# Kernel tuning notes

Hardware: AMD Instinct MI355X
Metric: run time of the kernel (lower is better)

The kernel has to match this reference:

```python
import jax, jax.numpy as jnp
import numpy as np

H = 8          # num heads
D = 16         # head dim
HID = 128      # hidden_dim = H * D
NM, ND, NA = 100000, 20000, 50000
E = 300000     # edges per relation
NUM_CLASSES = 8


def setup_inputs() -> dict:
    key = jax.random.key(0)
    ks = jax.random.split(key, 24)
    s = 0.05
    eye = jnp.eye(D, dtype=jnp.float32)
    inp = {
        'x_movie': jax.random.normal(ks[0], (NM, 256), jnp.float32),
        'x_director': jax.random.normal(ks[1], (ND, 128), jnp.float32),
        'x_actor': jax.random.normal(ks[2], (NA, 128), jnp.float32),
        # edge lists per relation: (director->movie, actor->movie, movie->director, movie->actor)
        'src_dm': jax.random.randint(ks[3], (E,), 0, ND),
        'dst_dm': jax.random.randint(ks[4], (E,), 0, NM),
        'src_am': jax.random.randint(ks[5], (E,), 0, NA),
        'dst_am': jax.random.randint(ks[6], (E,), 0, NM),
        'src_md': jax.random.randint(ks[7], (E,), 0, NM),
        'dst_md': jax.random.randint(ks[8], (E,), 0, ND),
        'src_ma': jax.random.randint(ks[9], (E,), 0, NM),
        'dst_ma': jax.random.randint(ks[10], (E,), 0, NA),
        # per-type pre-encoder (use_pre_encoder=True)
        'Wpre_m': jax.random.normal(ks[11], (256, HID), jnp.float32) * s,
        'Wpre_d': jax.random.normal(ks[12], (128, HID), jnp.float32) * s,
        'Wpre_a': jax.random.normal(ks[13], (128, HID), jnp.float32) * s,
        'bpre': jnp.zeros((3, HID), jnp.float32),
        # per-type K/Q/V projections, stacked over the 3 node types
        'Wk': jax.random.normal(ks[14], (3, HID, HID), jnp.float32) * s,
        'bk': jnp.zeros((3, HID), jnp.float32),
        'Wq': jax.random.normal(ks[15], (3, HID, HID), jnp.float32) * s,
        'bq': jnp.zeros((3, HID), jnp.float32),
        'Wv': jax.random.normal(ks[16], (3, HID, HID), jnp.float32) * s,
        'bv': jnp.zeros((3, HID), jnp.float32),
        # per-relation attention / message matrices and priors (4 relations)
        'a_rel': eye + jax.random.normal(ks[17], (4, H, D, D), jnp.float32) * s,
        'm_rel': eye + jax.random.normal(ks[18], (4, H, D, D), jnp.float32) * s,
        'p_rel': jnp.ones((4, H), jnp.float32),
        # per-type skip gate and output projection
        'skip': jnp.ones((3,), jnp.float32),
        'Wa': jax.random.normal(ks[19], (3, HID, HID), jnp.float32) * s,
        'ba': jnp.zeros((3, HID), jnp.float32),
        # final classification head on target node type ('movie')
        'Wlin': jax.random.normal(ks[20], (HID, NUM_CLASSES), jnp.float32) * s,
        'blin': jnp.zeros((NUM_CLASSES,), jnp.float32),
    }
    return inp


def _seg_softmax_agg(alpha, msg, dst, n):
    # softmax over incoming edges of each destination node, then weighted sum of msgs
    m = jax.ops.segment_max(alpha, dst, num_segments=n)      # [n, H]
    m = jnp.where(jnp.isfinite(m), m, 0.0)
    a = jnp.exp(alpha - m[dst])                              # [E, H]
    denom = jax.ops.segment_sum(a, dst, num_segments=n)      # [n, H]
    num = jax.ops.segment_sum(a[:, :, None] * msg, dst, num_segments=n)  # [n, H, D]
    return num / jnp.maximum(denom, 1e-16)[:, :, None]


def reference(x_movie, x_director, x_actor,
              src_dm, dst_dm, src_am, dst_am, src_md, dst_md, src_ma, dst_ma,
              Wpre_m, Wpre_d, Wpre_a, bpre, Wk, bk, Wq, bq, Wv, bv,
              a_rel, m_rel, p_rel, skip, Wa, ba, Wlin, blin):
    # type order: 0=movie, 1=director, 2=actor
    xs = [x_movie @ Wpre_m + bpre[0],
          x_director @ Wpre_d + bpre[1],
          x_actor @ Wpre_a + bpre[2]]
    k = [(x @ Wk[t] + bk[t]).reshape(-1, H, D) for t, x in enumerate(xs)]
    q = [(x @ Wq[t] + bq[t]).reshape(-1, H, D) for t, x in enumerate(xs)]
    v = [(x @ Wv[t] + bv[t]).reshape(-1, H, D) for t, x in enumerate(xs)]

    # (src_type, dst_type, src_idx, dst_idx) per relation
    rels = [(1, 0, src_dm, dst_dm), (2, 0, src_am, dst_am),
            (0, 1, src_md, dst_md), (0, 2, src_ma, dst_ma)]
    scale = 1.0 / np.sqrt(D).astype(np.float32)
    buckets = {0: [], 1: [], 2: []}
    for r, (st, dt, src, dst) in enumerate(rels):
        ke = jnp.einsum('ehd,hdf->ehf', k[st][src], a_rel[r])          # [E,H,D]
        al = jnp.einsum('ehf,ehf->eh', q[dt][dst], ke) * p_rel[r] * scale
        me = jnp.einsum('ehd,hdf->ehf', v[st][src], m_rel[r])          # [E,H,D]
        buckets[dt].append((al, me, dst))

    n = [x.shape[0] for x in xs]
    outs = []
    for t in range(3):
        al = jnp.concatenate([b[0] for b in buckets[t]], axis=0)
        me = jnp.concatenate([b[1] for b in buckets[t]], axis=0)
        dst = jnp.concatenate([b[2] for b in buckets[t]], axis=0)
        agg = _seg_softmax_agg(al, me, dst, n[t]).reshape(n[t], HID)
        h = jax.nn.gelu(agg, approximate=False) @ Wa[t] + ba[t]
        g = jax.nn.sigmoid(skip[t])
        outs.append(g * h + (1.0 - g) * xs[t])

    return outs[0] @ Wlin + blin
```

## Files before the change

### kernel.cpp

```cpp
#include <hip/hip_runtime.h>
#include <hip/hip_bf16.h>
#include <math.h>

#define NM 100000
#define ND 20000
#define NA 50000
#define EDG 300000
#define CAP 32

#define NT_M   3125
#define NT_D   625
#define NT_K   2188
#define T_M    7
#define T_K    7
#define BLK_M  447
#define BLK_K  313

typedef __attribute__((ext_vector_type(8))) short shortx8;
typedef __attribute__((ext_vector_type(4))) float floatx4;
typedef __attribute__((ext_vector_type(4))) int intx4;

__device__ __forceinline__ float bf2f(unsigned int u) {
    return __uint_as_float(u << 16);
}
__device__ __forceinline__ unsigned short f2bf(float f) {
    unsigned int x = __float_as_uint(f);
    unsigned int r = x + 0x7fffu + ((x >> 16) & 1u);
    return (unsigned short)(r >> 16);
}
__device__ __forceinline__ unsigned short f2bf_fast(float f) {
    return (unsigned short)((__float_as_uint(f) + 0x8000u) >> 16);
}
__device__ __forceinline__ unsigned int pkbf2(float a, float b) {
    return __builtin_amdgcn_perm(__float_as_uint(b) + 0x8000u,
                                 __float_as_uint(a) + 0x8000u,
                                 0x07060302u);
}
__device__ __forceinline__ float gelu_exact(float x) {
    return 0.5f * x * (1.0f + erff(x * 0.70710678118654752f));
}

static const size_t OFF_BT_Q      = 0;
static const size_t OFF_BT_KAMV_D = 73728;
static const size_t OFF_BT_KAMV_A = 139264;
static const size_t OFF_WKA_D     = 204800;
static const size_t OFF_WVM_D     = 270336;
static const size_t OFF_WKA_A     = 335872;
static const size_t OFF_WVM_A     = 401408;
static const size_t OFF_BQ        = 466944;
static const size_t OFF_B_KAMV_D  = 467520;
static const size_t OFF_B_KAMV_A  = 468544;
static const size_t OFF_BKA_D     = 469568;
static const size_t OFF_BVM_D     = 470080;
static const size_t OFF_BKA_A     = 470592;
static const size_t OFF_BVM_A     = 471104;
static const size_t OFF_WALS      = 471616;
static const size_t OFF_BFIN      = 475712;
static const size_t OFF_Q0        = 524288;
static const size_t OFF_SKIPB     = 26124288;
static const size_t OFF_WQT       = 26124288;
static const size_t OFF_KAMV_D    = 29324288;
static const size_t OFF_KAMV_A    = 39564288;
static const size_t OFF_COUNTS    = 65164288;
static const size_t OFF_SLOTS     = 65564288;
#define KAMV_A_DELTA 10240000

__global__ __launch_bounds__(256) void precompA(
    const float* __restrict__ Wk, const float* __restrict__ bk,
    const float* __restrict__ Wv, const float* __restrict__ bv,
    const float* __restrict__ Wa, const float* __restrict__ ba,
    const float* __restrict__ Wlin, const float* __restrict__ blin,
    const float* __restrict__ a_rel, const float* __restrict__ m_rel,
    const float* __restrict__ p_rel, const float* __restrict__ skip,
    const float* __restrict__ bpre, const float* __restrict__ Wq,
    char* __restrict__ ws)
{
    int tid = blockIdx.x * 256 + threadIdx.x;
    if (tid < 65536) {
        int mat = tid >> 14, rem = tid & 16383;
        int e = rem >> 7, hf = rem & 127, h = hf >> 4, f = hf & 15;
        const float* Wsrc; const float* R; float sc; float* dst;
        if (mat == 0)      { Wsrc = Wk + 16384; R = a_rel;        sc = p_rel[h]     * 0.25f; dst = (float*)(ws + OFF_WKA_D); }
        else if (mat == 1) { Wsrc = Wv + 16384; R = m_rel;        sc = 1.0f;                 dst = (float*)(ws + OFF_WVM_D); }
        else if (mat == 2) { Wsrc = Wk + 32768; R = a_rel + 2048; sc = p_rel[8 + h] * 0.25f; dst = (float*)(ws + OFF_WKA_A); }
        else               { Wsrc = Wv + 32768; R = m_rel + 2048; sc = 1.0f;                 dst = (float*)(ws + OFF_WVM_A); }
        float s = 0.0f;
        for (int d = 0; d < 16; d++)
            s += Wsrc[e * 128 + h * 16 + d] * R[h * 256 + d * 16 + f];
        dst[hf * 128 + e] = s * sc;
    } else if (tid < 66048) {
        int idx = tid - 65536;
        int mat = idx >> 7, hf = idx & 127, h = hf >> 4, f = hf & 15;
        const float* bsrc; const float* R; float sc; float* dst;
        if (mat == 0)      { bsrc = bk + 128; R = a_rel;        sc = p_rel[h]     * 0.25f; dst = (float*)(ws + OFF_BKA_D); }
        else if (mat == 1) { bsrc = bv + 128; R = m_rel;        sc = 1.0f;                 dst = (float*)(ws + OFF_BVM_D); }
        else if (mat == 2) { bsrc = bk + 256; R = a_rel + 2048; sc = p_rel[8 + h] * 0.25f; dst = (float*)(ws + OFF_BKA_A); }
        else               { bsrc = bv + 256; R = m_rel + 2048; sc = 1.0f;                 dst = (float*)(ws + OFF_BVM_A); }
        float s = 0.0f;
        for (int d = 0; d < 16; d++)
            s += bsrc[h * 16 + d] * R[h * 256 + d * 16 + f];
        dst[hf] = s * sc;
    } else if (tid < 67072) {
        int idx = tid - 66048;
        int j = idx >> 3, c = idx & 7;
        float g = 1.0f / (1.0f + __expf(-skip[0]));
        float s = 0.0f;
        for (int o = 0; o < 128; o++)
            s += Wa[j * 128 + o] * Wlin[o * 8 + c];
        ((float*)(ws + OFF_WALS))[j * 8 + c] = g * s;
    } else if (tid < 67080) {
        int c = tid - 67072;
        float g = 1.0f / (1.0f + __expf(-skip[0]));
        float s1 = 0.0f, s2 = 0.0f;
        for (int o = 0; o < 128; o++) {
            s1 += ba[o]   * Wlin[o * 8 + c];
            s2 += bpre[o] * Wlin[o * 8 + c];
        }
        ((float*)(ws + OFF_BFIN))[c] = g * s1 + (1.0f - g) * s2 + blin[c];
    } else if (tid < 83464) {
        int i = tid - 67080;
        int n = i >> 7, e = i & 127;
        ((float*)(ws + OFF_WQT))[n * 128 + e] = Wq[e * 128 + n];
    } else if (tid < 83464 + NM) {
        ((int*)(ws + OFF_COUNTS))[tid - 83464] = 0;
    }
}

__device__ __forceinline__ float dot128(const float* __restrict__ a,
                                        const float* __restrict__ b) {
    const floatx4* x = (const floatx4*)a;
    const floatx4* y = (const floatx4*)b;
    float s = 0.0f;
    #pragma unroll
    for (int i = 0; i < 32; i++) {
        floatx4 u = x[i], v = y[i];
        s += u[0] * v[0] + u[1] * v[1] + u[2] * v[2] + u[3] * v[3];
    }
    return s;
}

__global__ __launch_bounds__(256) void prep_scat(
    const int* __restrict__ src_dm, const int* __restrict__ dst_dm,
    const int* __restrict__ src_am, const int* __restrict__ dst_am,
    const float* __restrict__ Wpre_m, const float* __restrict__ Wpre_d,
    const float* __restrict__ Wpre_a, const float* __restrict__ bpre,
    const float* __restrict__ bq, const float* __restrict__ Wlin,
    const float* __restrict__ skip,
    char* __restrict__ ws)
{
    if (blockIdx.x < 2344) {
        int t = blockIdx.x * 256 + threadIdx.x;
        if (t >= 2 * EDG) return;
        int src, dst, delta;
        if (t < EDG) { src = src_dm[t];       dst = dst_dm[t];       delta = 0; }
        else         { src = src_am[t - EDG]; dst = dst_am[t - EDG]; delta = KAMV_A_DELTA; }
        int* counts = (int*)(ws + OFF_COUNTS);
        int* slots  = (int*)(ws + OFF_SLOTS);
        int pos = atomicAdd(&counts[dst], 1);
        if (pos < CAP) slots[(size_t)dst * CAP + pos] = src * 512 + delta;
        return;
    }
    int tid = (blockIdx.x - 2344) * 256 + threadIdx.x;
    const float* WKA_D = (const float*)(ws + OFF_WKA_D);
    const float* WVM_D = (const float*)(ws + OFF_WVM_D);
    const float* WKA_A = (const float*)(ws + OFF_WKA_A);
    const float* WVM_A = (const float*)(ws + OFF_WVM_A);
    const float* WqT   = (const float*)(ws + OFF_WQT);

    if (tid < 36864) {
        int n = tid >> 8, c = tid & 255;
        float s = 0.0f;
        if (n < 128) {
            s = dot128(Wpre_m + c * 128, WqT + n * 128);
        } else if (n < 136) {
            int cc = n - 128;
            float g = 1.0f / (1.0f + __expf(-skip[0]));
            for (int e = 0; e < 128; e++)
                s += Wpre_m[c * 128 + e] * Wlin[e * 8 + cc];
            s *= (1.0f - g);
        }
        ((unsigned short*)(ws + OFF_BT_Q))[(c >> 7) * 18432 + n * 128 + (c & 127)] = f2bf(s);
    } else if (tid < 69632) {
        int idx = tid - 36864;
        int nrow = idx >> 7, c = idx & 127;
        const float* WfT = (nrow < 128) ? WKA_D : WVM_D;
        int nc = nrow & 127;
        float s = dot128(Wpre_d + c * 128, WfT + nc * 128);
        ((unsigned short*)(ws + OFF_BT_KAMV_D))[nrow * 128 + c] = f2bf(s);
    } else if (tid < 102400) {
        int idx = tid - 69632;
        int nrow = idx >> 7, c = idx & 127;
        const float* WfT = (nrow < 128) ? WKA_A : WVM_A;
        int nc = nrow & 127;
        float s = dot128(Wpre_a + c * 128, WfT + nc * 128);
        ((unsigned short*)(ws + OFF_BT_KAMV_A))[nrow * 128 + c] = f2bf(s);
    } else if (tid < 102544) {
        int n = tid - 102400;
        float s = 0.0f;
        if (n < 128) s = dot128(bpre, WqT + n * 128) + bq[n];
        ((float*)(ws + OFF_BQ))[n] = s;
    } else if (tid < 102800) {
        int nrow = tid - 102544;
        const float* WfT = (nrow < 128) ? WKA_D : WVM_D;
        const float* bf_ = (nrow < 128) ? (const float*)(ws + OFF_BKA_D) : (const float*)(ws + OFF_BVM_D);
        int nc = nrow & 127;
        ((float*)(ws + OFF_B_KAMV_D))[nrow] = dot128(bpre + 128, WfT + nc * 128) + bf_[nc];
    } else if (tid < 103056) {
        int nrow = tid - 102800;
        const float* WfT = (nrow < 128) ? WKA_A : WVM_A;
        const float* bf_ = (nrow < 128) ? (const float*)(ws + OFF_BKA_A) : (const float*)(ws + OFF_BVM_A);
        int nc = nrow & 127;
        ((float*)(ws + OFF_B_KAMV_A))[nrow] = dot128(bpre + 256, WfT + nc * 128) + bf_[nc];
    }
}

#define MFMA16(a, b, c) __builtin_amdgcn_mfma_f32_16x16x32_bf16(a, b, c, 0, 0, 0)

__global__ __launch_bounds__(256, 3) void gemm_all(
    const float* __restrict__ xm, const float* __restrict__ xd,
    const float* __restrict__ xa,
    const unsigned short* __restrict__ btq,
    const unsigned short* __restrict__ btd,
    const unsigned short* __restrict__ bta,
    const float* __restrict__ bq,
    const float* __restrict__ bbd, const float* __restrict__ bba,
    unsigned short* __restrict__ q0, float* __restrict__ skipb,
    unsigned short* __restrict__ outd, unsigned short* __restrict__ outa)
{
    __shared__ unsigned short a_lds[32 * 136];
    __shared__ unsigned short b_lds[144 * 136];
    int tid = threadIdx.x;
    int w = tid >> 6, lane = tid & 63;
    int quad = lane >> 4, low = lane & 15;
    int g = w >> 1, s = w & 1;
    int bx = blockIdx.x;

    if (bx < BLK_M) {
        int tbase = bx * T_M;
        floatx4 av[4];
        intx4 bv[9];
        {
            int row0 = (tbase < NT_M ? tbase : NT_M - 1) * 32;
            #pragma unroll
            for (int it = 0; it < 4; it++) {
                int f = it * 256 + tid, r = f >> 5, c4 = f & 31;
                av[it] = *(const floatx4*)(xm + (size_t)(row0 + r) * 256 + c4 * 4);
            }
            #pragma unroll
            for (int it = 0; it < 9; it++) {
                int idx = it * 256 + tid, n = idx >> 4, ch = idx & 15;
                bv[it] = *(const intx4*)&btq[(size_t)n * 128 + ch * 8];
            }
        }
        for (int t = 0; t < T_M; t++) {
            int tcur = tbase + t;
            if (tcur >= NT_M) break;
            int row0 = tcur * 32;
            floatx4 acc[5] = {};
            #pragma unroll
            for (int h = 0; h < 2; h++) {
                __syncthreads();
                #pragma unroll
                for (int it = 0; it < 4; it++) {
                    int f = it * 256 + tid, r = f >> 5, c4 = f & 31;
                    unsigned long long d =
                        ((unsigned long long)pkbf2(av[it][2], av[it][3]) << 32) |
                        pkbf2(av[it][0], av[it][1]);
                    *(unsigned long long*)&a_lds[r * 136 + c4 * 4] = d;
                }
                #pragma unroll
                for (int it = 0; it < 9; it++) {
                    int idx = it * 256 + tid, n = idx >> 4, ch = idx & 15;
                    *(intx4*)&b_lds[n * 136 + ch * 8] = bv[it];
                }
                __syncthreads();
                {
                    int ntile = (h == 0) ? tcur : (tcur + 1 < NT_M ? tcur + 1 : NT_M - 1);
                    int nh = 1 - h;
                    int nrow0 = ntile * 32;
                    #pragma unroll
                    for (int it = 0; it < 4; it++) {
                        int f = it * 256 + tid, r = f >> 5, c4 = f & 31;
                        av[it] = *(const floatx4*)(xm + (size_t)(nrow0 + r) * 256 + nh * 128 + c4 * 4);
                    }
                    #pragma unroll
                    for (int it = 0; it < 9; it++) {
                        int idx = it * 256 + tid, n = idx >> 4, ch = idx & 15;
                        bv[it] = *(const intx4*)&btq[(size_t)nh * 18432 + n * 128 + ch * 8];
                    }
                }
                #pragma unroll
                for (int ks = 0; ks < 4; ks++) {
                    int ko = ks * 32 + quad * 8;
                    shortx8 a0 = *(const shortx8*)&a_lds[(s * 16 + low) * 136 + ko];
                    #pragma unroll
                    for (int j = 0; j < 5; j++) {
                        if (g == 1 && j == 4) continue;
                        int nt = g * 5 + j;
                        shortx8 b = *(const shortx8*)&b_lds[(nt * 16 + low) * 136 + ko];
                        acc[j] = MFMA16(a0, b, acc[j]);
                    }
                }
            }
            #pragma unroll
            for (int j = 0; j < 5; j++) {
                if (g == 1 && j == 4) continue;
                int nt = g * 5 + j;
                int col = nt * 16 + low;
                #pragma unroll
                for (int r = 0; r < 4; r++) {
                    int row = row0 + s * 16 + quad * 4 + r;
                    float v = acc[j][r] + bq[col];
                    if (nt == 8) {
                        if (low < 8) skipb[(size_t)row * 8 + low] = v;
                    } else {
                        q0[(size_t)row * 128 + col] = f2bf_fast(v);
                    }
                }
            }
        }
    } else {
        int kbase = (bx - BLK_M) * T_K;
        floatx4 av[4];
        intx4 bv[8];
        {
            int tt = kbase < NT_K ? kbase : NT_K - 1;
            const float* A; int M, row0;
            const unsigned short* BT;
            if (tt < NT_D) { A = xd; M = ND; row0 = tt * 32; BT = btd; }
            else           { A = xa; M = NA; row0 = (tt - NT_D) * 32; BT = bta; }
            #pragma unroll
            for (int it = 0; it < 4; it++) {
                int f = it * 256 + tid, r = f >> 5, c4 = f & 31;
                int rg = row0 + r; if (rg >= M) rg = M - 1;
                av[it] = *(const floatx4*)(A + (size_t)rg * 128 + c4 * 4);
            }
            #pragma unroll
            for (int it = 0; it < 8; it++) {
                int idx = it * 256 + tid, n = idx >> 4, ch = idx & 15;
                bv[it] = *(const intx4*)&BT[(size_t)n * 128 + ch * 8];
            }
        }
        for (int t = 0; t < T_K; t++) {
            int tcur = kbase + t;
            if (tcur >= NT_K) break;
            const float* A; int M, row0;
            const unsigned short* BT; const float* bias;
            unsigned short* outb;
            if (tcur < NT_D) { A = xd; M = ND; row0 = tcur * 32; BT = btd; bias = bbd; outb = outd; }
            else             { A = xa; M = NA; row0 = (tcur - NT_D) * 32; BT = bta; bias = bba; outb = outa; }

            #pragma unroll
            for (int pnl = 0; pnl < 2; pnl++) {
                __syncthreads();
                if (pnl == 0) {
                    #pragma unroll
                    for (int it = 0; it < 4; it++) {
                        int f = it * 256 + tid, r = f >> 5, c4 = f & 31;
                        unsigned long long d =
                            ((unsigned long long)pkbf2(av[it][2], av[it][3]) << 32) |
                            pkbf2(av[it][0], av[it][1]);
                        *(unsigned long long*)&a_lds[r * 136 + c4 * 4] = d;
                    }
                }
                #pragma unroll
                for (int it = 0; it < 8; it++) {
                    int idx = it * 256 + tid, n = idx >> 4, ch = idx & 15;
                    *(intx4*)&b_lds[n * 136 + ch * 8] = bv[it];
                }
                __syncthreads();
                if (pnl == 0) {
                    #pragma unroll
                    for (int it = 0; it < 8; it++) {
                        int idx = it * 256 + tid, n = idx >> 4, ch = idx & 15;
                        bv[it] = *(const intx4*)&BT[16384 + (size_t)n * 128 + ch * 8];
                    }
                } else {
                    int tn = (tcur + 1 < NT_K) ? tcur + 1 : NT_K - 1;
                    const float* An; int Mn, nrow0;
                    const unsigned short* BTn;
                    if (tn < NT_D) { An = xd; Mn = ND; nrow0 = tn * 32; BTn = btd; }
                    else           { An = xa; Mn = NA; nrow0 = (tn - NT_D) * 32; BTn = bta; }
                    #pragma unroll
                    for (int it = 0; it < 4; it++) {
                        int f = it * 256 + tid, r = f >> 5, c4 = f & 31;
                        int rg = nrow0 + r; if (rg >= Mn) rg = Mn - 1;
                        av[it] = *(const floatx4*)(An + (size_t)rg * 128 + c4 * 4);
                    }
                    #pragma unroll
                    for (int it = 0; it < 8; it++) {
                        int idx = it * 256 + tid, n = idx >> 4, ch = idx & 15;
                        bv[it] = *(const intx4*)&BTn[(size_t)n * 128 + ch * 8];
                    }
                }
                floatx4 acc[4] = {};
                #pragma unroll
                for (int ks = 0; ks < 4; ks++) {
                    int ko = ks * 32 + quad * 8;
                    shortx8 a0 = *(const shortx8*)&a_lds[(s * 16 + low) * 136 + ko];
                    #pragma unroll
                    for (int j = 0; j < 4; j++) {
                        int nt = g * 4 + j;
                        shortx8 b = *(const shortx8*)&b_lds[(nt * 16 + low) * 136 + ko];
                        acc[j] = MFMA16(a0, b, acc[j]);
                    }
                }
                #pragma unroll
                for (int j = 0; j < 4; j++) {
                    int nt = g * 4 + j;
                    int col = pnl * 128 + nt * 16 + low;
                    #pragma unroll
                    for (int r = 0; r < 4; r++) {
                        int row = row0 + s * 16 + quad * 4 + r;
                        if (row < M)
                            outb[(size_t)row * 256 + col] = f2bf_fast(acc[j][r] + bias[pnl * 128 + nt * 16 + low]);
                    }
                }
            }
        }
    }
}

__global__ __launch_bounds__(256) void agg_kernel(
    const unsigned short* __restrict__ q0,
    const char* __restrict__ kamv0,
    const int* __restrict__ counts, const int* __restrict__ slots,
    const float* __restrict__ skipb,
    const float* __restrict__ WaLs, const float* __restrict__ bfin,
    float* __restrict__ out)
{
    __shared__ float wals[1032];
    for (int i = threadIdx.x; i < 1024; i += 256) {
        int c = i >> 7, rem = i & 127, j = rem >> 4, L = rem & 15;
        wals[i] = WaLs[(L * 8 + j) * 8 + c];
    }
    if (threadIdx.x < 8) wals[1024 + threadIdx.x] = bfin[threadIdx.x];
    __syncthreads();

    int lane = threadIdx.x & 63;
    int grp = lane >> 4;
    int L   = lane & 15;
    int n = blockIdx.x * 16 + (threadIdx.x >> 6) * 4 + grp;

    intx4 qv = *(const intx4*)(q0 + (size_t)n * 128 + L * 8);
    float qf[8];
    #pragma unroll
    for (int d = 0; d < 4; d++) {
        unsigned int u = (unsigned int)qv[d];
        qf[2 * d]     = __uint_as_float(u << 16);
        qf[2 * d + 1] = __uint_as_float(u & 0xffff0000u);
    }

    int cnt = counts[n];
    cnt = cnt < 0 ? 0 : (cnt > CAP ? CAP : cnt);
    int s0 = slots[(size_t)n * CAP + L];

    float acc[8] = {0, 0, 0, 0, 0, 0, 0, 0};
    float den = 0.0f;
    if (cnt > 0) {
        int off0 = __shfl(s0, lane & 48);
        const char* p = kamv0 + off0;
        intx4 ku = *(const intx4*)(p + L * 16);
        intx4 mu = *(const intx4*)(p + 256 + L * 16);
        for (int i = 0; i < cnt; i++) {
            int inext = (i + 1 < cnt) ? i + 1 : i;
            int offn = __shfl(s0, (lane & 48) + (inext & 15));
            if (__builtin_expect(inext >= 16, 0)) offn = slots[(size_t)n * CAP + inext];
            const char* pn = kamv0 + offn;
            intx4 kun = *(const intx4*)(pn + L * 16);
            intx4 mun = *(const intx4*)(pn + 256 + L * 16);

            float ph = 0.0f;
            #pragma unroll
            for (int d = 0; d < 4; d++) {
                unsigned int u = (unsigned int)ku[d];
                ph += qf[2 * d]     * __uint_as_float(u << 16);
                ph += qf[2 * d + 1] * __uint_as_float(u & 0xffff0000u);
            }
            float pf = ph + __shfl_xor(ph, 1);
            float wgt = __expf(fminf(pf, 60.0f));
            den += wgt;
            #pragma unroll
            for (int d = 0; d < 4; d++) {
                unsigned int u = (unsigned int)mu[d];
                acc[2 * d]     += wgt * __uint_as_float(u << 16);
                acc[2 * d + 1] += wgt * __uint_as_float(u & 0xffff0000u);
            }
            ku = kun; mu = mun;
        }
    }
    float inv = 1.0f / fmaxf(den, 1e-16f);

    float part[8] = {0, 0, 0, 0, 0, 0, 0, 0};
    #pragma unroll
    for (int j = 0; j < 8; j++) {
        float u = gelu_exact(acc[j] * inv);
        #pragma unroll
        for (int c = 0; c < 8; c++)
            part[c] += u * wals[c * 128 + j * 16 + L];
    }

    bool b0 = lane & 1, b1 = lane & 2, b2 = lane & 4;
    float t1[4], t2[2], t3;
    #pragma unroll
    for (int k = 0; k < 4; k++) {
        float send = b0 ? part[k] : part[4 + k];
        float got  = __shfl_xor(send, 1);
        t1[k] = (b0 ? part[4 + k] : part[k]) + got;
    }
    #pragma unroll
    for (int k = 0; k < 2; k++) {
        float send = b1 ? t1[k] : t1[2 + k];
        float got  = __shfl_xor(send, 2);
        t2[k] = (b1 ? t1[2 + k] : t1[k]) + got;
    }
    {
        float send = b2 ? t2[0] : t2[1];
        float got  = __shfl_xor(send, 4);
        t3 = (b2 ? t2[1] : t2[0]) + got;
    }
    t3 += __shfl_xor(t3, 8);
    if (L < 8) {
        int c = 4 * (L & 1) + 2 * ((L >> 1) & 1) + ((L >> 2) & 1);
        out[(size_t)n * 8 + c] = t3 + skipb[(size_t)n * 8 + c] + wals[1024 + c];
    }
}

extern "C" void kernel_launch(void* const* d_in, const int* in_sizes, int n_in,
                              void* d_out, int out_size, void* d_ws, size_t ws_size,
                              hipStream_t stream) {
    (void)in_sizes; (void)n_in; (void)out_size; (void)ws_size;
    const float* x_movie    = (const float*)d_in[0];
    const float* x_director = (const float*)d_in[1];
    const float* x_actor    = (const float*)d_in[2];
    const int* src_dm = (const int*)d_in[3];
    const int* dst_dm = (const int*)d_in[4];
    const int* src_am = (const int*)d_in[5];
    const int* dst_am = (const int*)d_in[6];
    const float* Wpre_m = (const float*)d_in[11];
    const float* Wpre_d = (const float*)d_in[12];
    const float* Wpre_a = (const float*)d_in[13];
    const float* bpre   = (const float*)d_in[14];
    const float* Wk     = (const float*)d_in[15];
    const float* bk     = (const float*)d_in[16];
    const float* Wq     = (const float*)d_in[17];
    const float* bq     = (const float*)d_in[18];
    const float* Wv     = (const float*)d_in[19];
    const float* bv     = (const float*)d_in[20];
    const float* a_rel  = (const float*)d_in[21];
    const float* m_rel  = (const float*)d_in[22];
    const float* p_rel  = (const float*)d_in[23];
    const float* skip   = (const float*)d_in[24];
    const float* Wa     = (const float*)d_in[25];
    const float* ba     = (const float*)d_in[26];
    const float* Wlin   = (const float*)d_in[27];
    const float* blin   = (const float*)d_in[28];

    char* ws = (char*)d_ws;
    float* out = (float*)d_out;

    precompA<<<(83464 + NM + 255) / 256, 256, 0, stream>>>(
        Wk, bk, Wv, bv, Wa, ba, Wlin, blin,
        a_rel, m_rel, p_rel, skip, bpre, Wq, ws);

    prep_scat<<<2344 + 403, 256, 0, stream>>>(
        src_dm, dst_dm, src_am, dst_am,
        Wpre_m, Wpre_d, Wpre_a, bpre, bq, Wlin, skip, ws);

    gemm_all<<<BLK_M + BLK_K, 256, 0, stream>>>(
        x_movie, x_director, x_actor,
        (const unsigned short*)(ws + OFF_BT_Q),
        (const unsigned short*)(ws + OFF_BT_KAMV_D),
        (const unsigned short*)(ws + OFF_BT_KAMV_A),
        (const float*)(ws + OFF_BQ),
        (const float*)(ws + OFF_B_KAMV_D), (const float*)(ws + OFF_B_KAMV_A),
        (unsigned short*)(ws + OFF_Q0), (float*)(ws + OFF_SKIPB),
        (unsigned short*)(ws + OFF_KAMV_D), (unsigned short*)(ws + OFF_KAMV_A));

    agg_kernel<<<NM / 16, 256, 0, stream>>>(
        (const unsigned short*)(ws + OFF_Q0),
        (const char*)(ws + OFF_KAMV_D),
        (const int*)(ws + OFF_COUNTS), (const int*)(ws + OFF_SLOTS),
        (const float*)(ws + OFF_SKIPB),
        (const float*)(ws + OFF_WALS), (const float*)(ws + OFF_BFIN), out);
}
```

Before: 402.2 us.

## Keep full weight matrix resident in LDS and feed A fragments from registers

The projection GEMM now loads the entire bf16 weight panel into shared memory once per block. Each wave then independently processes four 16-row tiles, loading A rows straight from global memory into registers, packing them to bf16 and feeding the MFMA without staging through LDS. This removes the per-tile barriers and LDS writes of A and re-staging of B, and register prefetch of the next tile overlaps loads with compute. The cost is a larger LDS footprint and more registers (occupancy hint lowered from 3 to 2), and the director and actor blocks are now split statically.

```diff
diff --git a/kernel.cpp b/kernel.cpp
--- a/kernel.cpp
+++ b/kernel.cpp
@@ -8,13 +8,12 @@
 #define EDG 300000
 #define CAP 32
 
-#define NT_M   3125
-#define NT_D   625
-#define NT_K   2188
-#define T_M    7
-#define T_K    7
-#define BLK_M  447
-#define BLK_K  313
+#define NTM 6250
+#define NTD 1250
+#define NTA 3125
+#define MB  391
+#define DB  79
+#define AB  196
 
 typedef __attribute__((ext_vector_type(8))) short shortx8;
 typedef __attribute__((ext_vector_type(4))) float floatx4;
@@ -35,6 +34,14 @@
     return __builtin_amdgcn_perm(__float_as_uint(b) + 0x8000u,
                                  __float_as_uint(a) + 0x8000u,
                                  0x07060302u);
+}
+__device__ __forceinline__ shortx8 pack8(floatx4 a, floatx4 b) {
+    intx4 r;
+    r[0] = (int)pkbf2(a[0], a[1]);
+    r[1] = (int)pkbf2(a[2], a[3]);
+    r[2] = (int)pkbf2(b[0], b[1]);
+    r[3] = (int)pkbf2(b[2], b[3]);
+    return __builtin_bit_cast(shortx8, r);
 }
 __device__ __forceinline__ float gelu_exact(float x) {
     return 0.5f * x * (1.0f + erff(x * 0.70710678118654752f));
@@ -216,7 +223,7 @@
 
 #define MFMA16(a, b, c) __builtin_amdgcn_mfma_f32_16x16x32_bf16(a, b, c, 0, 0, 0)
 
-__global__ __launch_bounds__(256, 3) void gemm_all(
+__global__ __launch_bounds__(256, 2) void gemm_all(
     const float* __restrict__ xm, const float* __restrict__ xd,
     const float* __restrict__ xa,
     const unsigned short* __restrict__ btq,
@@ -227,194 +234,136 @@
     unsigned short* __restrict__ q0, float* __restrict__ skipb,
     unsigned short* __restrict__ outd, unsigned short* __restrict__ outa)
 {
-    __shared__ unsigned short a_lds[32 * 136];
-    __shared__ unsigned short b_lds[144 * 136];
+    __shared__ unsigned short b_lds[288 * 136];
     int tid = threadIdx.x;
     int w = tid >> 6, lane = tid & 63;
     int quad = lane >> 4, low = lane & 15;
-    int g = w >> 1, s = w & 1;
     int bx = blockIdx.x;
 
-    if (bx < BLK_M) {
-        int tbase = bx * T_M;
-        floatx4 av[4];
-        intx4 bv[9];
+    if (bx < MB) {
+        #pragma unroll
+        for (int it = 0; it < 18; it++) {
+            int idx = it * 256 + tid, r = idx >> 4, ch = idx & 15;
+            *(intx4*)&b_lds[r * 136 + ch * 8] =
+                *(const intx4*)&btq[(size_t)r * 128 + ch * 8];
+        }
+        __syncthreads();
+        float bqr[9];
+        #pragma unroll
+        for (int j = 0; j < 9; j++) bqr[j] = bq[j * 16 + low];
+
+        int t0 = (bx * 4 + w) * 4;
+        floatx4 st[16];
         {
-            int row0 = (tbase < NT_M ? tbase : NT_M - 1) * 32;
-            #pragma unroll
-            for (int it = 0; it < 4; it++) {
-                int f = it * 256 + tid, r = f >> 5, c4 = f & 31;
-                av[it] = *(const floatx4*)(xm + (size_t)(row0 + r) * 256 + c4 * 4);
-            }
-            #pragma unroll
-            for (int it = 0; it < 9; it++) {
-                int idx = it * 256 + tid, n = idx >> 4, ch = idx & 15;
-                bv[it] = *(const intx4*)&btq[(size_t)n * 128 + ch * 8];
-            }
-        }
-        for (int t = 0; t < T_M; t++) {
-            int tcur = tbase + t;
-            if (tcur >= NT_M) break;
-            int row0 = tcur * 32;
-            floatx4 acc[5] = {};
-            #pragma unroll
-            for (int h = 0; h < 2; h++) {
-                __syncthreads();
+            int te = t0 < NTM ? t0 : NTM - 1;
+            const float* Ap = xm + (size_t)(te * 16 + low) * 256 + quad * 8;
+            #pragma unroll
+            for (int ks = 0; ks < 8; ks++) {
+                st[2 * ks]     = *(const floatx4*)(Ap + ks * 32);
+                st[2 * ks + 1] = *(const floatx4*)(Ap + ks * 32 + 4);
+            }
+        }
+        #pragma unroll
+        for (int i = 0; i < 4; i++) {
+            int t = t0 + i;
+            shortx8 fa[8];
+            #pragma unroll
+            for (int ks = 0; ks < 8; ks++) fa[ks] = pack8(st[2 * ks], st[2 * ks + 1]);
+            {
+                int tn = t + 1 < NTM ? t + 1 : NTM - 1;
+                const float* Ap = xm + (size_t)(tn * 16 + low) * 256 + quad * 8;
                 #pragma unroll
-                for (int it = 0; it < 4; it++) {
-                    int f = it * 256 + tid, r = f >> 5, c4 = f & 31;
-                    unsigned long long d =
-                        ((unsigned long long)pkbf2(av[it][2], av[it][3]) << 32) |
-                        pkbf2(av[it][0], av[it][1]);
-                    *(unsigned long long*)&a_lds[r * 136 + c4 * 4] = d;
-                }
+                for (int ks = 0; ks < 8; ks++) {
+                    st[2 * ks]     = *(const floatx4*)(Ap + ks * 32);
+                    st[2 * ks + 1] = *(const floatx4*)(Ap + ks * 32 + 4);
+                }
+            }
+            floatx4 acc[9] = {};
+            #pragma unroll
+            for (int ks = 0; ks < 8; ks++) {
+                int rb = (ks >> 2) * 19584 + low * 136 + (ks & 3) * 32 + quad * 8;
                 #pragma unroll
-                for (int it = 0; it < 9; it++) {
-                    int idx = it * 256 + tid, n = idx >> 4, ch = idx & 15;
-                    *(intx4*)&b_lds[n * 136 + ch * 8] = bv[it];
-                }
-                __syncthreads();
-                {
-                    int ntile = (h == 0) ? tcur : (tcur + 1 < NT_M ? tcur + 1 : NT_M - 1);
-                    int nh = 1 - h;
-                    int nrow0 = ntile * 32;
+                for (int j = 0; j < 9; j++) {
+                    shortx8 b = *(const shortx8*)&b_lds[rb + j * 2176];
+                    acc[j] = MFMA16(fa[ks], b, acc[j]);
+                }
+            }
+            if (t < NTM) {
+                int row0 = t * 16 + quad * 4;
+                #pragma unroll
+                for (int j = 0; j < 8; j++) {
+                    int col = j * 16 + low;
                     #pragma unroll
-                    for (int it = 0; it < 4; it++) {
-                        int f = it * 256 + tid, r = f >> 5, c4 = f & 31;
-                        av[it] = *(const floatx4*)(xm + (size_t)(nrow0 + r) * 256 + nh * 128 + c4 * 4);
-                    }
+                    for (int r = 0; r < 4; r++)
+                        q0[(size_t)(row0 + r) * 128 + col] = f2bf_fast(acc[j][r] + bqr[j]);
+                }
+                if (low < 8) {
                     #pragma unroll
-                    for (int it = 0; it < 9; it++) {
-                        int idx = it * 256 + tid, n = idx >> 4, ch = idx & 15;
-                        bv[it] = *(const intx4*)&btq[(size_t)nh * 18432 + n * 128 + ch * 8];
-                    }
-                }
+                    for (int r = 0; r < 4; r++)
+                        skipb[(size_t)(row0 + r) * 8 + low] = acc[8][r] + bqr[8];
+                }
+            }
+        }
+    } else {
+        const float* A; const unsigned short* BT; const float* bias;
+        unsigned short* outb; int ntt, wid;
+        if (bx < MB + DB) { A = xd; BT = btd; bias = bbd; outb = outd; ntt = NTD; wid = (bx - MB) * 4 + w; }
+        else              { A = xa; BT = bta; bias = bba; outb = outa; ntt = NTA; wid = (bx - MB - DB) * 4 + w; }
+        #pragma unroll
+        for (int it = 0; it < 16; it++) {
+            int idx = it * 256 + tid, r = idx >> 4, ch = idx & 15;
+            *(intx4*)&b_lds[r * 136 + ch * 8] =
+                *(const intx4*)&BT[(size_t)r * 128 + ch * 8];
+        }
+        __syncthreads();
+        float biasr[16];
+        #pragma unroll
+        for (int j = 0; j < 16; j++) biasr[j] = bias[j * 16 + low];
+
+        int t0 = wid * 4;
+        floatx4 st[8];
+        {
+            int te = t0 < ntt ? t0 : ntt - 1;
+            const float* Ap = A + (size_t)(te * 16 + low) * 128 + quad * 8;
+            #pragma unroll
+            for (int ks = 0; ks < 4; ks++) {
+                st[2 * ks]     = *(const floatx4*)(Ap + ks * 32);
+                st[2 * ks + 1] = *(const floatx4*)(Ap + ks * 32 + 4);
+            }
+        }
+        #pragma unroll
+        for (int i = 0; i < 4; i++) {
+            int t = t0 + i;
+            shortx8 fa[4];
+            #pragma unroll
+            for (int ks = 0; ks < 4; ks++) fa[ks] = pack8(st[2 * ks], st[2 * ks + 1]);
+            {
+                int tn = t + 1 < ntt ? t + 1 : ntt - 1;
+                const float* Ap = A + (size_t)(tn * 16 + low) * 128 + quad * 8;
                 #pragma unroll
                 for (int ks = 0; ks < 4; ks++) {
-                    int ko = ks * 32 + quad * 8;
-                    shortx8 a0 = *(const shortx8*)&a_lds[(s * 16 + low) * 136 + ko];
+                    st[2 * ks]     = *(const floatx4*)(Ap + ks * 32);
+                    st[2 * ks + 1] = *(const floatx4*)(Ap + ks * 32 + 4);
+                }
+            }
+            floatx4 acc[16] = {};
+            #pragma unroll
+            for (int ks = 0; ks < 4; ks++) {
+                int rb = low * 136 + ks * 32 + quad * 8;
+                #pragma unroll
+                for (int j = 0; j < 16; j++) {
+                    shortx8 b = *(const shortx8*)&b_lds[rb + j * 2176];
+                    acc[j] = MFMA16(fa[ks], b, acc[j]);
+                }
+            }
+            if (t < ntt) {
+                int row0 = t * 16 + quad * 4;
+                #pragma unroll
+                for (int j = 0; j < 16; j++) {
+                    int col = j * 16 + low;
                     #pragma unroll
-                    for (int j = 0; j < 5; j++) {
-                        if (g == 1 && j == 4) continue;
-                        int nt = g * 5 + j;
-                        shortx8 b = *(const shortx8*)&b_lds[(nt * 16 + low) * 136 + ko];
-                        acc[j] = MFMA16(a0, b, acc[j]);
-                    }
-                }
-            }
-            #pragma unroll
-            for (int j = 0; j < 5; j++) {
-                if (g == 1 && j == 4) continue;
-                int nt = g * 5 + j;
-                int col = nt * 16 + low;
-                #pragma unroll
-                for (int r = 0; r < 4; r++) {
-                    int row = row0 + s * 16 + quad * 4 + r;
-                    float v = acc[j][r] + bq[col];
-                    if (nt == 8) {
-                        if (low < 8) skipb[(size_t)row * 8 + low] = v;
-                    } else {
-                        q0[(size_t)row * 128 + col] = f2bf_fast(v);
-                    }
-                }
-            }
-        }
-    } else {
-        int kbase = (bx - BLK_M) * T_K;
-        floatx4 av[4];
-        intx4 bv[8];
-        {
-            int tt = kbase < NT_K ? kbase : NT_K - 1;
-            const float* A; int M, row0;
-            const unsigned short* BT;
-            if (tt < NT_D) { A = xd; M = ND; row0 = tt * 32; BT = btd; }
-            else           { A = xa; M = NA; row0 = (tt - NT_D) * 32; BT = bta; }
-            #pragma unroll
-            for (int it = 0; it < 4; it++) {
-                int f = it * 256 + tid, r = f >> 5, c4 = f & 31;
-                int rg = row0 + r; if (rg >= M) rg = M - 1;
-                av[it] = *(const floatx4*)(A + (size_t)rg * 128 + c4 * 4);
-            }
-            #pragma unroll
-            for (int it = 0; it < 8; it++) {
-                int idx = it * 256 + tid, n = idx >> 4, ch = idx & 15;
-                bv[it] = *(const intx4*)&BT[(size_t)n * 128 + ch * 8];
-            }
-        }
-        for (int t = 0; t < T_K; t++) {
-            int tcur = kbase + t;
-            if (tcur >= NT_K) break;
-            const float* A; int M, row0;
-            const unsigned short* BT; const float* bias;
-            unsigned short* outb;
-            if (tcur < NT_D) { A = xd; M = ND; row0 = tcur * 32; BT = btd; bias = bbd; outb = outd; }
-            else             { A = xa; M = NA; row0 = (tcur - NT_D) * 32; BT = bta; bias = bba; outb = outa; }
-
-            #pragma unroll
-            for (int pnl = 0; pnl < 2; pnl++) {
-                __syncthreads();
-                if (pnl == 0) {
-                    #pragma unroll
-                    for (int it = 0; it < 4; it++) {
-                        int f = it * 256 + tid, r = f >> 5, c4 = f & 31;
-                        unsigned long long d =
-                            ((unsigned long long)pkbf2(av[it][2], av[it][3]) << 32) |
-                            pkbf2(av[it][0], av[it][1]);
-                        *(unsigned long long*)&a_lds[r * 136 + c4 * 4] = d;
-                    }
-                }
-                #pragma unroll
-                for (int it = 0; it < 8; it++) {
-                    int idx = it * 256 + tid, n = idx >> 4, ch = idx & 15;
-                    *(intx4*)&b_lds[n * 136 + ch * 8] = bv[it];
-                }
-                __syncthreads();
-                if (pnl == 0) {
-                    #pragma unroll
-                    for (int it = 0; it < 8; it++) {
-                        int idx = it * 256 + tid, n = idx >> 4, ch = idx & 15;
-                        bv[it] = *(const intx4*)&BT[16384 + (size_t)n * 128 + ch * 8];
-                    }
-                } else {
-                    int tn = (tcur + 1 < NT_K) ? tcur + 1 : NT_K - 1;
-                    const float* An; int Mn, nrow0;
-                    const unsigned short* BTn;
-                    if (tn < NT_D) { An = xd; Mn = ND; nrow0 = tn * 32; BTn = btd; }
-                    else           { An = xa; Mn = NA; nrow0 = (tn - NT_D) * 32; BTn = bta; }
-                    #pragma unroll
-                    for (int it = 0; it < 4; it++) {
-                        int f = it * 256 + tid, r = f >> 5, c4 = f & 31;
-                        int rg = nrow0 + r; if (rg >= Mn) rg = Mn - 1;
-                        av[it] = *(const floatx4*)(An + (size_t)rg * 128 + c4 * 4);
-                    }
-                    #pragma unroll
-                    for (int it = 0; it < 8; it++) {
-                        int idx = it * 256 + tid, n = idx >> 4, ch = idx & 15;
-                        bv[it] = *(const intx4*)&BTn[(size_t)n * 128 + ch * 8];
-                    }
-                }
-                floatx4 acc[4] = {};
-                #pragma unroll
-                for (int ks = 0; ks < 4; ks++) {
-                    int ko = ks * 32 + quad * 8;
-                    shortx8 a0 = *(const shortx8*)&a_lds[(s * 16 + low) * 136 + ko];
-                    #pragma unroll
-                    for (int j = 0; j < 4; j++) {
-                        int nt = g * 4 + j;
-                        shortx8 b = *(const shortx8*)&b_lds[(nt * 16 + low) * 136 + ko];
-                        acc[j] = MFMA16(a0, b, acc[j]);
-                    }
-                }
-                #pragma unroll
-                for (int j = 0; j < 4; j++) {
-                    int nt = g * 4 + j;
-                    int col = pnl * 128 + nt * 16 + low;
-                    #pragma unroll
-                    for (int r = 0; r < 4; r++) {
-                        int row = row0 + s * 16 + quad * 4 + r;
-                        if (row < M)
-                            outb[(size_t)row * 256 + col] = f2bf_fast(acc[j][r] + bias[pnl * 128 + nt * 16 + low]);
-                    }
+                    for (int r = 0; r < 4; r++)
+                        outb[(size_t)(row0 + r) * 256 + col] = f2bf_fast(acc[j][r] + biasr[j]);
                 }
             }
         }
@@ -567,7 +516,7 @@
         src_dm, dst_dm, src_am, dst_am,
         Wpre_m, Wpre_d, Wpre_a, bpre, bq, Wlin, skip, ws);
 
-    gemm_all<<<BLK_M + BLK_K, 256, 0, stream>>>(
+    gemm_all<<<MB + DB + AB, 256, 0, stream>>>(
         x_movie, x_director, x_actor,
         (const unsigned short*)(ws + OFF_BT_Q),
         (const unsigned short*)(ws + OFF_BT_KAMV_D),
```

Measured after the change: 377.3 us. 6.2% less time.
